# Performance work log

Hardware: AMD Instinct MI355X
Metric: run time of the kernel (lower is better)

The kernel has to match this reference:

```python
import jax, jax.numpy as jnp
import numpy as np

N, E, D = 50000, 800000, 128

def setup_inputs() -> dict:
    key = jax.random.key(0)
    ks = jax.random.split(key, 10)
    s = 0.05
    return {
        "h": jax.random.normal(ks[0], (N, D), dtype=jnp.float32),
        "coords": jax.random.normal(ks[1], (N, 3), dtype=jnp.float32),
        "edge_index": jax.random.randint(ks[2], (2, E), 0, N, dtype=jnp.int64),
        "W1": jax.random.normal(ks[3], (D, 2 * D + 1), dtype=jnp.float32) * s,
        "b1": jnp.zeros((D,), dtype=jnp.float32),
        "W2": jax.random.normal(ks[4], (D, D), dtype=jnp.float32) * s,
        "b2": jnp.zeros((D,), dtype=jnp.float32),
        "U1": jax.random.normal(ks[5], (D, 2 * D), dtype=jnp.float32) * s,
        "c1": jnp.zeros((D,), dtype=jnp.float32),
        "U2": jax.random.normal(ks[6], (D, D), dtype=jnp.float32) * s,
        "c2": jnp.zeros((D,), dtype=jnp.float32),
    }


def reference(h, coords, edge_index, W1, b1, W2, b2, U1, c1, U2, c2):
    sender, receiver = edge_index[0], edge_index[1]
    # gather endpoints
    rel = coords[sender] - coords[receiver]                  # [E, 3]
    dist = jnp.linalg.norm(rel, axis=1, keepdims=True)       # [E, 1]
    m_in = jnp.concatenate([h[sender], h[receiver], dist], axis=1)  # [E, 2D+1]
    # message MLP (Linear -> SiLU -> Linear -> SiLU)
    m = jax.nn.silu(m_in @ W1.T + b1)
    m = jax.nn.silu(m @ W2.T + b2)                           # [E, D]
    # scatter-add aggregate into receivers
    agg = jax.ops.segment_sum(m, receiver, num_segments=h.shape[0])  # [N, D]
    # update MLP (Linear -> SiLU -> Linear) with residual
    u_in = jnp.concatenate([h, agg], axis=1)                 # [N, 2D]
    u = jax.nn.silu(u_in @ U1.T + c1)
    u = u @ U2.T + c2
    return h + u
```

## Files before the change

### kernel.cpp

```cpp
#include <hip/hip_runtime.h>
#include <hip/hip_bf16.h>

#define NN 50000
#define EE 800000
#define DD 128
#define NTILES_MAX 100000

typedef __attribute__((ext_vector_type(8))) short bf16x8;
typedef __attribute__((ext_vector_type(4))) float f32x4;

__device__ __forceinline__ short f2bf(float f) {
    __hip_bfloat16 h = __float2bfloat16(f);
    return __builtin_bit_cast(short, h);
}

__device__ __forceinline__ float bf2f(short s) {
    unsigned int u = ((unsigned int)(unsigned short)s) << 16;
    return __builtin_bit_cast(float, u);
}

__device__ __forceinline__ float fast_silu(float x) {
    return x * __builtin_amdgcn_rcpf(1.0f + __expf(-x));
}

__device__ __forceinline__ bf16x8 load_frag_f32(const float* p) {
    f32x4 a = *(const f32x4*)p;
    f32x4 b = *(const f32x4*)(p + 4);
    bf16x8 t;
    t[0] = f2bf(a[0]); t[1] = f2bf(a[1]); t[2] = f2bf(a[2]); t[3] = f2bf(a[3]);
    t[4] = f2bf(b[0]); t[5] = f2bf(b[1]); t[6] = f2bf(b[2]); t[7] = f2bf(b[3]);
    return t;
}

__global__ void prep_all_kernel(const int* __restrict__ ei, int* __restrict__ cnt,
                                const float* __restrict__ W1, const float* __restrict__ W2,
                                const float* __restrict__ U1, const float* __restrict__ U2,
                                unsigned short* __restrict__ packs,
                                float* __restrict__ w1c_out) {
    if (blockIdx.x < 3125) {
        int e = blockIdx.x * 256 + threadIdx.x;
        atomicAdd(&cnt[ei[EE + e]], 1);
        return;
    }
    int t = (blockIdx.x - 3125) * blockDim.x + threadIdx.x;
    if (t >= 98304) {
        if (t < 98432) { int d = t - 98304; w1c_out[d] = W1[d * 257 + 256]; }
        return;
    }
    int mat = t >> 14;
    int r = t & 16383;
    int j = r & 7;
    int lane = (r >> 3) & 63;
    int f = r >> 9;
    int ks = f & 3, nt = f >> 2;
    int n = nt * 16 + (lane & 15);
    int k = ks * 32 + (lane >> 4) * 8 + j;
    float v;
    switch (mat) {
        case 0: v = W1[n * 257 + k];        break;
        case 1: v = W1[n * 257 + 128 + k];  break;
        case 2: v = W2[n * 128 + k];        break;
        case 3: v = U1[n * 256 + k];        break;
        case 4: v = U1[n * 256 + 128 + k];  break;
        default: v = U2[n * 128 + k];       break;
    }
    packs[t] = (unsigned short)f2bf(v);
}

__global__ void alloc_kernel(const int* __restrict__ cnt, int* __restrict__ tileCtr,
                             int* __restrict__ cursor, int2* __restrict__ tinfo,
                             float4* __restrict__ agg4) {
    int i = blockIdx.x * 256 + threadIdx.x;
    if (i >= NN) return;
    int c = cnt[i];
    int ntt = (c + 15) >> 4;
    if (ntt == 0) ntt = 1;
    int tb = atomicAdd(tileCtr, ntt);
    int base = tb << 4;
    cursor[i] = base;
    int end = base + c;
    if (ntt == 1) {
        tinfo[tb] = make_int2(i | (int)0x80000000, end);
    } else {
        for (int k = 0; k < ntt; k++) tinfo[tb + k] = make_int2(i, end);
        float4* row = agg4 + (size_t)i * 32;
        #pragma unroll 8
        for (int k = 0; k < 32; k++) row[k] = make_float4(0.f, 0.f, 0.f, 0.f);
    }
}

__global__ __launch_bounds__(256, 2) void prep_g_scatter_kernel(
    const float* __restrict__ h,
    const bf16x8* __restrict__ w1a_pack,
    const bf16x8* __restrict__ w1b_pack,
    const float* __restrict__ b1,
    unsigned short* __restrict__ G,
    const int* __restrict__ ei,
    int* __restrict__ cursor,
    int* __restrict__ ssr)
{
    if (blockIdx.x >= 782) {
        int e = (blockIdx.x - 782) * 256 + threadIdx.x;
        int s = ei[e], r = ei[EE + e];
        int pos = atomicAdd(&cursor[r], 1);
        ssr[pos] = s;
        return;
    }
    const int tid = threadIdx.x;
    const int wave = tid >> 6, lane = tid & 63;
    const int quad = lane >> 4, l15 = lane & 15;
    const int nbase = blockIdx.x * 64 + wave * 16;

    int n = nbase + l15;
    int nrow = n < NN ? n : NN - 1;

    bf16x8 ah[4];
    #pragma unroll
    for (int ks = 0; ks < 4; ks++)
        ah[ks] = load_frag_f32(h + (size_t)nrow * DD + ks * 32 + quad * 8);

    f32x4 acca[8], accb[8];
    #pragma unroll
    for (int nt = 0; nt < 8; nt++) {
        acca[nt] = f32x4{0.f, 0.f, 0.f, 0.f};
        accb[nt] = f32x4{0.f, 0.f, 0.f, 0.f};
    }

    #pragma unroll
    for (int ks = 0; ks < 4; ks++) {
        #pragma unroll
        for (int nt = 0; nt < 8; nt++)
            acca[nt] = __builtin_amdgcn_mfma_f32_16x16x32_bf16(
                ah[ks], w1a_pack[(nt * 4 + ks) * 64 + lane], acca[nt], 0, 0, 0);
        #pragma unroll
        for (int nt = 0; nt < 8; nt++)
            accb[nt] = __builtin_amdgcn_mfma_f32_16x16x32_bf16(
                ah[ks], w1b_pack[(nt * 4 + ks) * 64 + lane], accb[nt], 0, 0, 0);
    }

    #pragma unroll
    for (int nt = 0; nt < 8; nt++) {
        int d = nt * 16 + l15;
        float b1v = b1[d];
        #pragma unroll
        for (int r = 0; r < 4; r++) {
            int n2 = nbase + quad * 4 + r;
            if (n2 < NN) {
                G[(size_t)n2 * 256 + d]       = (unsigned short)f2bf(acca[nt][r] + b1v);
                G[(size_t)n2 * 256 + 128 + d] = (unsigned short)f2bf(accb[nt][r]);
            }
        }
    }
}

__global__ __launch_bounds__(256, 4) void edge_kernel(
    const unsigned short* __restrict__ G,
    const float* __restrict__ coords,
    const int* __restrict__ ssr,
    const int2* __restrict__ tinfo,
    const int* __restrict__ tileCtr,
    const bf16x8* __restrict__ w2_pack,
    const float* __restrict__ w1c,
    const float* __restrict__ b2,
    float* __restrict__ agg)
{
    __shared__ float w1c_s[4][128];

    const int tid = threadIdx.x;
    const int wave = tid >> 6, lane = tid & 63;
    const int quad = lane >> 4, l15 = lane & 15;

    w1c_s[wave][lane] = w1c[lane];
    w1c_s[wave][64 + lane] = w1c[64 + lane];
    asm volatile("s_waitcnt lgkmcnt(0)" ::: "memory");

    float b2f[8];
    #pragma unroll
    for (int nt = 0; nt < 8; nt++) b2f[nt] = b2[nt * 16 + l15];

    const int ntot = *tileCtr;
    const int tbase = (blockIdx.x * 4 + wave) * 4;

    #pragma unroll
    for (int mt = 0; mt < 4; mt++) {
        const int t = tbase + mt;
        if (t >= ntot) continue;

        const int2 ti = tinfo[t];
        const bool single = ti.x < 0;
        const int rnode = ti.x & 0x7FFFFFFF;
        const int end = ti.y;
        const int slot0 = t * 16;
        const bool fullt = (slot0 + 16 <= end);

        bf16x8 gb[4];
        #pragma unroll
        for (int ks = 0; ks < 4; ks++)
            gb[ks] = *(const bf16x8*)(G + (size_t)rnode * 256 + 128 + ks * 32 + quad * 8);
        float rx = coords[3 * rnode + 0];
        float ry = coords[3 * rnode + 1];
        float rz = coords[3 * rnode + 2];

        int sraw = ssr[slot0 + l15];
        int sc = fullt ? sraw
                       : ((slot0 + l15 < end) ? sraw : rnode);

        bf16x8 ga[4];
        #pragma unroll
        for (int ks = 0; ks < 4; ks++)
            ga[ks] = *(const bf16x8*)(G + (size_t)sc * 256 + ks * 32 + quad * 8);
        float dx = coords[3 * sc + 0] - rx;
        float dy = coords[3 * sc + 1] - ry;
        float dz = coords[3 * sc + 2] - rz;
        float dist = sqrtf(dx * dx + dy * dy + dz * dz);

        bf16x8 m1f[4];
        #pragma unroll
        for (int ks = 0; ks < 4; ks++) {
            f32x4 c0 = *(const f32x4*)&w1c_s[wave][ks * 32 + quad * 8];
            f32x4 c1 = *(const f32x4*)&w1c_s[wave][ks * 32 + quad * 8 + 4];
            #pragma unroll
            for (int j = 0; j < 4; j++) {
                float pre0 = bf2f(ga[ks][j])     + bf2f(gb[ks][j])     + dist * c0[j];
                float pre1 = bf2f(ga[ks][4 + j]) + bf2f(gb[ks][4 + j]) + dist * c1[j];
                m1f[ks][j]     = f2bf(fast_silu(pre0));
                m1f[ks][4 + j] = f2bf(fast_silu(pre1));
            }
        }

        f32x4 sv[8];
        #pragma unroll
        for (int nt = 0; nt < 8; nt++) sv[nt] = f32x4{0.f, 0.f, 0.f, 0.f};
        #pragma unroll
        for (int ks = 0; ks < 4; ks++)
            #pragma unroll
            for (int nt = 0; nt < 8; nt++)
                sv[nt] = __builtin_amdgcn_mfma_f32_16x16x32_bf16(
                    m1f[ks], w2_pack[(nt * 4 + ks) * 64 + lane], sv[nt], 0, 0, 0);

        float acc[8];
        #pragma unroll
        for (int nt = 0; nt < 8; nt++) acc[nt] = 0.f;
        if (fullt) {
            #pragma unroll
            for (int nt = 0; nt < 8; nt++)
                #pragma unroll
                for (int r = 0; r < 4; r++)
                    acc[nt] += fast_silu(sv[nt][r] + b2f[nt]);
        } else {
            float mk[4];
            #pragma unroll
            for (int r = 0; r < 4; r++)
                mk[r] = (slot0 + quad * 4 + r < end) ? 1.f : 0.f;
            #pragma unroll
            for (int nt = 0; nt < 8; nt++)
                #pragma unroll
                for (int r = 0; r < 4; r++) {
                    float v = fast_silu(sv[nt][r] + b2f[nt]);
                    acc[nt] = fmaf(v, mk[r], acc[nt]);
                }
        }

        #pragma unroll
        for (int nt = 0; nt < 8; nt++) {
            float s = acc[nt];
            s += __shfl_xor(s, 16);
            s += __shfl_xor(s, 32);
            acc[nt] = s;
        }
        size_t base = (size_t)rnode * DD + l15;
        if (single) {
            agg[base + (quad * 2 + 0) * 16] = acc[quad * 2 + 0];
            agg[base + (quad * 2 + 1) * 16] = acc[quad * 2 + 1];
        } else {
            unsafeAtomicAdd(&agg[base + (quad * 2 + 0) * 16], acc[quad * 2 + 0]);
            unsafeAtomicAdd(&agg[base + (quad * 2 + 1) * 16], acc[quad * 2 + 1]);
        }
    }
}

__global__ __launch_bounds__(256, 4) void node_kernel(
    const float* __restrict__ hf,
    const float* __restrict__ agg,
    const bf16x8* __restrict__ u1a_pack,
    const bf16x8* __restrict__ u1b_pack,
    const bf16x8* __restrict__ u2_pack,
    const float* __restrict__ c1,
    const float* __restrict__ c2,
    float* __restrict__ out)
{
    __shared__ unsigned short u1s[4][16][136];

    const int tid = threadIdx.x;
    const int wave = tid >> 6, lane = tid & 63;
    const int quad = lane >> 4, l15 = lane & 15;
    const int nbase = blockIdx.x * 64 + wave * 16;

    int n = nbase + l15;
    int nrow = n < NN ? n : NN - 1;

    float c1v[8];
    #pragma unroll
    for (int nt = 0; nt < 8; nt++) c1v[nt] = c1[nt * 16 + l15];

    bf16x8 ah[4], ag[4];
    #pragma unroll
    for (int ks = 0; ks < 4; ks++) {
        ah[ks] = load_frag_f32(hf + (size_t)nrow * DD + ks * 32 + quad * 8);
        ag[ks] = load_frag_f32(agg + (size_t)nrow * DD + ks * 32 + quad * 8);
    }

    f32x4 acc[8];
    #pragma unroll
    for (int nt = 0; nt < 8; nt++) acc[nt] = f32x4{0.f, 0.f, 0.f, 0.f};

    #pragma unroll
    for (int ks = 0; ks < 4; ks++) {
        #pragma unroll
        for (int nt = 0; nt < 8; nt++)
            acc[nt] = __builtin_amdgcn_mfma_f32_16x16x32_bf16(
                ah[ks], u1a_pack[(nt * 4 + ks) * 64 + lane], acc[nt], 0, 0, 0);
        #pragma unroll
        for (int nt = 0; nt < 8; nt++)
            acc[nt] = __builtin_amdgcn_mfma_f32_16x16x32_bf16(
                ag[ks], u1b_pack[(nt * 4 + ks) * 64 + lane], acc[nt], 0, 0, 0);
    }

    #pragma unroll
    for (int nt = 0; nt < 8; nt++) {
        int d = nt * 16 + l15;
        #pragma unroll
        for (int r = 0; r < 4; r++) {
            float pre = acc[nt][r] + c1v[nt];
            u1s[wave][quad * 4 + r][d] = (unsigned short)f2bf(fast_silu(pre));
        }
    }
    asm volatile("s_waitcnt lgkmcnt(0)" ::: "memory");

    bf16x8 a2[4];
    #pragma unroll
    for (int ks = 0; ks < 4; ks++)
        a2[ks] = *(const bf16x8*)(&u1s[wave][l15][ks * 32 + quad * 8]);

    f32x4 acc2[8];
    #pragma unroll
    for (int nt = 0; nt < 8; nt++) acc2[nt] = f32x4{0.f, 0.f, 0.f, 0.f};

    #pragma unroll
    for (int ks = 0; ks < 4; ks++)
        #pragma unroll
        for (int nt = 0; nt < 8; nt++)
            acc2[nt] = __builtin_amdgcn_mfma_f32_16x16x32_bf16(
                a2[ks], u2_pack[(nt * 4 + ks) * 64 + lane], acc2[nt], 0, 0, 0);

    #pragma unroll
    for (int nt = 0; nt < 8; nt++) {
        int d = nt * 16 + l15;
        float c2v = c2[d];
        #pragma unroll
        for (int r = 0; r < 4; r++) {
            int n2 = nbase + quad * 4 + r;
            if (n2 < NN) {
                size_t idx = (size_t)n2 * DD + d;
                out[idx] = hf[idx] + acc2[nt][r] + c2v;
            }
        }
    }
}

extern "C" void kernel_launch(void* const* d_in, const int* in_sizes, int n_in,
                              void* d_out, int out_size, void* d_ws, size_t ws_size,
                              hipStream_t stream) {
    const float* h      = (const float*)d_in[0];
    const float* coords = (const float*)d_in[1];
    const int* ei       = (const int*)d_in[2];
    const float* W1 = (const float*)d_in[3];
    const float* b1 = (const float*)d_in[4];
    const float* W2 = (const float*)d_in[5];
    const float* b2 = (const float*)d_in[6];
    const float* U1 = (const float*)d_in[7];
    const float* c1 = (const float*)d_in[8];
    const float* U2 = (const float*)d_in[9];
    const float* c2 = (const float*)d_in[10];
    float* out = (float*)d_out;

    char* ws = (char*)d_ws;
    float* agg            = (float*)ws;
    unsigned short* packs = (unsigned short*)(ws + 38400000);
    float* w1c            = (float*)(ws + 38600000);
    unsigned short* G     = (unsigned short*)(ws + 38700000);
    int* cnt              = (int*)(ws + 64300000);
    int* tileCtr          = (int*)(ws + 64500000);
    int* cursor           = (int*)(ws + 64500008);
    int2* tinfo           = (int2*)(ws + 64700008);
    int* ssr              = (int*)(ws + 65500008);
    const bf16x8* w1a = (const bf16x8*)(packs);
    const bf16x8* w1b = (const bf16x8*)(packs + 16384);
    const bf16x8* w2p = (const bf16x8*)(packs + 32768);
    const bf16x8* u1a = (const bf16x8*)(packs + 49152);
    const bf16x8* u1b = (const bf16x8*)(packs + 65536);
    const bf16x8* u2p = (const bf16x8*)(packs + 81920);

    hipMemsetAsync(cnt, 0, 200004, stream);
    prep_all_kernel<<<3510, 256, 0, stream>>>(ei, cnt, W1, W2, U1, U2, packs, w1c);
    alloc_kernel<<<196, 256, 0, stream>>>(cnt, tileCtr, cursor, tinfo, (float4*)agg);
    prep_g_scatter_kernel<<<3907, 256, 0, stream>>>(h, w1a, w1b, b1, G, ei,
                                                    cursor, ssr);
    edge_kernel<<<6250, 256, 0, stream>>>(G, coords, ssr, tinfo, tileCtr,
                                          w2p, w1c, b2, agg);
    node_kernel<<<(NN + 63) / 64, 256, 0, stream>>>(h, agg, u1a, u1b, u2p, c1, c2, out);
}
```

Before: 390.5 us.

## Pack partial receiver tiles into shared tail pool to cut padded edge tiles

Each receiver's edges are split into full 16-edge tiles and a remainder. Remainders from all receivers go into a compacted (sender, receiver) pool, which is processed in dense 16-row tiles that do a segmented reduction by receiver before the atomic adds. The goal is to drop the padding waste of one partial tile per node: about 100k padded tiles become about 50k dense ones, so the edge grid halves. In exchange, tail tiles load per-row receiver features, use a serial segmented reduce with more atomics, and agg now needs a full memset instead of direct stores for single-tile nodes.

```diff
diff --git a/kernel.cpp b/kernel.cpp
--- a/kernel.cpp
+++ b/kernel.cpp
@@ -4,7 +4,6 @@
 #define NN 50000
 #define EE 800000
 #define DD 128
-#define NTILES_MAX 100000
 
 typedef __attribute__((ext_vector_type(8))) short bf16x8;
 typedef __attribute__((ext_vector_type(4))) float f32x4;
@@ -67,26 +66,19 @@
     packs[t] = (unsigned short)f2bf(v);
 }
 
-__global__ void alloc_kernel(const int* __restrict__ cnt, int* __restrict__ tileCtr,
-                             int* __restrict__ cursor, int2* __restrict__ tinfo,
-                             float4* __restrict__ agg4) {
+__global__ void alloc_kernel(const int* __restrict__ cnt, int* __restrict__ ctrs,
+                             int* __restrict__ fullbase, int* __restrict__ tailbase,
+                             int* __restrict__ tinfoA) {
     int i = blockIdx.x * 256 + threadIdx.x;
     if (i >= NN) return;
     int c = cnt[i];
-    int ntt = (c + 15) >> 4;
-    if (ntt == 0) ntt = 1;
-    int tb = atomicAdd(tileCtr, ntt);
-    int base = tb << 4;
-    cursor[i] = base;
-    int end = base + c;
-    if (ntt == 1) {
-        tinfo[tb] = make_int2(i | (int)0x80000000, end);
-    } else {
-        for (int k = 0; k < ntt; k++) tinfo[tb + k] = make_int2(i, end);
-        float4* row = agg4 + (size_t)i * 32;
-        #pragma unroll 8
-        for (int k = 0; k < 32; k++) row[k] = make_float4(0.f, 0.f, 0.f, 0.f);
-    }
+    int nf = c >> 4, tc = c & 15;
+    if (nf) {
+        int tb = atomicAdd(&ctrs[0], nf);
+        fullbase[i] = tb << 4;
+        for (int k = 0; k < nf; k++) tinfoA[tb + k] = i;
+    }
+    if (tc) tailbase[i] = atomicAdd(&ctrs[1], tc);
 }
 
 __global__ __launch_bounds__(256, 2) void prep_g_scatter_kernel(
@@ -96,14 +88,20 @@
     const float* __restrict__ b1,
     unsigned short* __restrict__ G,
     const int* __restrict__ ei,
+    const int* __restrict__ cnt,
     int* __restrict__ cursor,
-    int* __restrict__ ssr)
+    const int* __restrict__ fullbase,
+    const int* __restrict__ tailbase,
+    int* __restrict__ ssrA,
+    int2* __restrict__ pool)
 {
     if (blockIdx.x >= 782) {
         int e = (blockIdx.x - 782) * 256 + threadIdx.x;
         int s = ei[e], r = ei[EE + e];
-        int pos = atomicAdd(&cursor[r], 1);
-        ssr[pos] = s;
+        int p = atomicAdd(&cursor[r], 1);
+        int thr = cnt[r] & ~15;
+        if (p < thr) ssrA[fullbase[r] + p] = s;
+        else         pool[tailbase[r] + p - thr] = make_int2(s, r);
         return;
     }
     const int tid = threadIdx.x;
@@ -156,9 +154,10 @@
 __global__ __launch_bounds__(256, 4) void edge_kernel(
     const unsigned short* __restrict__ G,
     const float* __restrict__ coords,
-    const int* __restrict__ ssr,
-    const int2* __restrict__ tinfo,
-    const int* __restrict__ tileCtr,
+    const int* __restrict__ ssrA,
+    const int2* __restrict__ pool,
+    const int* __restrict__ tinfoA,
+    const int* __restrict__ ctrs,
     const bf16x8* __restrict__ w2_pack,
     const float* __restrict__ w1c,
     const float* __restrict__ b2,
@@ -178,41 +177,54 @@
     #pragma unroll
     for (int nt = 0; nt < 8; nt++) b2f[nt] = b2[nt * 16 + l15];
 
-    const int ntot = *tileCtr;
+    const int nfullT = ctrs[0];
+    const int ntail  = ctrs[1];
+    const int ntiles = nfullT + ((ntail + 15) >> 4);
     const int tbase = (blockIdx.x * 4 + wave) * 4;
 
     #pragma unroll
     for (int mt = 0; mt < 4; mt++) {
         const int t = tbase + mt;
-        if (t >= ntot) continue;
-
-        const int2 ti = tinfo[t];
-        const bool single = ti.x < 0;
-        const int rnode = ti.x & 0x7FFFFFFF;
-        const int end = ti.y;
-        const int slot0 = t * 16;
-        const bool fullt = (slot0 + 16 <= end);
-
-        bf16x8 gb[4];
-        #pragma unroll
-        for (int ks = 0; ks < 4; ks++)
-            gb[ks] = *(const bf16x8*)(G + (size_t)rnode * 256 + 128 + ks * 32 + quad * 8);
-        float rx = coords[3 * rnode + 0];
-        float ry = coords[3 * rnode + 1];
-        float rz = coords[3 * rnode + 2];
-
-        int sraw = ssr[slot0 + l15];
-        int sc = fullt ? sraw
-                       : ((slot0 + l15 < end) ? sraw : rnode);
-
-        bf16x8 ga[4];
-        #pragma unroll
-        for (int ks = 0; ks < 4; ks++)
-            ga[ks] = *(const bf16x8*)(G + (size_t)sc * 256 + ks * 32 + quad * 8);
-        float dx = coords[3 * sc + 0] - rx;
-        float dy = coords[3 * sc + 1] - ry;
-        float dz = coords[3 * sc + 2] - rz;
-        float dist = sqrtf(dx * dx + dy * dy + dz * dz);
+        if (t >= ntiles) continue;
+
+        const bool full = t < nfullT;
+        bf16x8 ga[4], gb[4];
+        float dist;
+        int rnode = 0;
+        int rr = 0;
+
+        if (full) {
+            rnode = tinfoA[t];
+            #pragma unroll
+            for (int ks = 0; ks < 4; ks++)
+                gb[ks] = *(const bf16x8*)(G + (size_t)rnode * 256 + 128 + ks * 32 + quad * 8);
+            float rx = coords[3 * rnode + 0];
+            float ry = coords[3 * rnode + 1];
+            float rz = coords[3 * rnode + 2];
+            int sc = ssrA[t * 16 + l15];
+            #pragma unroll
+            for (int ks = 0; ks < 4; ks++)
+                ga[ks] = *(const bf16x8*)(G + (size_t)sc * 256 + ks * 32 + quad * 8);
+            float dx = coords[3 * sc + 0] - rx;
+            float dy = coords[3 * sc + 1] - ry;
+            float dz = coords[3 * sc + 2] - rz;
+            dist = sqrtf(dx * dx + dy * dy + dz * dz);
+        } else {
+            const int pbase = (t - nfullT) * 16;
+            int slot = pbase + l15;
+            int cl = slot < ntail ? slot : ntail - 1;
+            int2 sd = pool[cl];
+            int sc = sd.x; rr = sd.y;
+            #pragma unroll
+            for (int ks = 0; ks < 4; ks++) {
+                ga[ks] = *(const bf16x8*)(G + (size_t)sc * 256 + ks * 32 + quad * 8);
+                gb[ks] = *(const bf16x8*)(G + (size_t)rr * 256 + 128 + ks * 32 + quad * 8);
+            }
+            float dx = coords[3 * sc + 0] - coords[3 * rr + 0];
+            float dy = coords[3 * sc + 1] - coords[3 * rr + 1];
+            float dz = coords[3 * sc + 2] - coords[3 * rr + 2];
+            dist = sqrtf(dx * dx + dy * dy + dz * dz);
+        }
 
         bf16x8 m1f[4];
         #pragma unroll
@@ -238,43 +250,56 @@
                 sv[nt] = __builtin_amdgcn_mfma_f32_16x16x32_bf16(
                     m1f[ks], w2_pack[(nt * 4 + ks) * 64 + lane], sv[nt], 0, 0, 0);
 
-        float acc[8];
-        #pragma unroll
-        for (int nt = 0; nt < 8; nt++) acc[nt] = 0.f;
-        if (fullt) {
-            #pragma unroll
-            for (int nt = 0; nt < 8; nt++)
+        if (full) {
+            float acc[8];
+            #pragma unroll
+            for (int nt = 0; nt < 8; nt++) {
+                float s = 0.f;
                 #pragma unroll
                 for (int r = 0; r < 4; r++)
-                    acc[nt] += fast_silu(sv[nt][r] + b2f[nt]);
+                    s += fast_silu(sv[nt][r] + b2f[nt]);
+                s += __shfl_xor(s, 16);
+                s += __shfl_xor(s, 32);
+                acc[nt] = s;
+            }
+            size_t base = (size_t)rnode * DD + l15;
+            unsafeAtomicAdd(&agg[base + (quad * 2 + 0) * 16], acc[quad * 2 + 0]);
+            unsafeAtomicAdd(&agg[base + (quad * 2 + 1) * 16], acc[quad * 2 + 1]);
         } else {
-            float mk[4];
-            #pragma unroll
-            for (int r = 0; r < 4; r++)
-                mk[r] = (slot0 + quad * 4 + r < end) ? 1.f : 0.f;
+            const int pbase = (t - nfullT) * 16;
             #pragma unroll
             for (int nt = 0; nt < 8; nt++)
                 #pragma unroll
                 for (int r = 0; r < 4; r++) {
                     float v = fast_silu(sv[nt][r] + b2f[nt]);
-                    acc[nt] = fmaf(v, mk[r], acc[nt]);
+                    sv[nt][r] = (pbase + quad * 4 + r < ntail) ? v : 0.f;
                 }
-        }
-
-        #pragma unroll
-        for (int nt = 0; nt < 8; nt++) {
-            float s = acc[nt];
-            s += __shfl_xor(s, 16);
-            s += __shfl_xor(s, 32);
-            acc[nt] = s;
-        }
-        size_t base = (size_t)rnode * DD + l15;
-        if (single) {
-            agg[base + (quad * 2 + 0) * 16] = acc[quad * 2 + 0];
-            agg[base + (quad * 2 + 1) * 16] = acc[quad * 2 + 1];
-        } else {
-            unsafeAtomicAdd(&agg[base + (quad * 2 + 0) * 16], acc[quad * 2 + 0]);
-            unsafeAtomicAdd(&agg[base + (quad * 2 + 1) * 16], acc[quad * 2 + 1]);
+            int nxt = __shfl(rr, (l15 + 1) & 15);
+            unsigned long long bal = __ballot(l15 == 15 || rr != nxt);
+            unsigned m = (unsigned)(bal & 0xFFFFull);
+            int i0 = 0;
+            while (m) {
+                int b = (int)__builtin_ctz(m);
+                m &= m - 1;
+                float tot[8];
+                #pragma unroll
+                for (int nt = 0; nt < 8; nt++) {
+                    float s = 0.f;
+                    #pragma unroll
+                    for (int r = 0; r < 4; r++) {
+                        int row = quad * 4 + r;
+                        s += (row >= i0 && row <= b) ? sv[nt][r] : 0.f;
+                    }
+                    s += __shfl_xor(s, 16);
+                    s += __shfl_xor(s, 32);
+                    tot[nt] = s;
+                }
+                int rcv = __shfl(rr, i0);
+                size_t base = (size_t)rcv * DD + l15;
+                unsafeAtomicAdd(&agg[base + (quad * 2 + 0) * 16], tot[quad * 2 + 0]);
+                unsafeAtomicAdd(&agg[base + (quad * 2 + 1) * 16], tot[quad * 2 + 1]);
+                i0 = b + 1;
+            }
         }
     }
 }
@@ -390,10 +415,13 @@
     float* w1c            = (float*)(ws + 38600000);
     unsigned short* G     = (unsigned short*)(ws + 38700000);
     int* cnt              = (int*)(ws + 64300000);
-    int* tileCtr          = (int*)(ws + 64500000);
-    int* cursor           = (int*)(ws + 64500008);
-    int2* tinfo           = (int2*)(ws + 64700008);
-    int* ssr              = (int*)(ws + 65500008);
+    int* cursor           = (int*)(ws + 64500000);
+    int* ctrs             = (int*)(ws + 64700000);
+    int* fullbase         = (int*)(ws + 64700008);
+    int* tailbase         = (int*)(ws + 64900008);
+    int* tinfoA           = (int*)(ws + 65100008);
+    int* ssrA             = (int*)(ws + 65300008);
+    int2* pool            = (int2*)(ws + 68500008);
     const bf16x8* w1a = (const bf16x8*)(packs);
     const bf16x8* w1b = (const bf16x8*)(packs + 16384);
     const bf16x8* w2p = (const bf16x8*)(packs + 32768);
@@ -401,12 +429,14 @@
     const bf16x8* u1b = (const bf16x8*)(packs + 65536);
     const bf16x8* u2p = (const bf16x8*)(packs + 81920);
 
-    hipMemsetAsync(cnt, 0, 200004, stream);
+    hipMemsetAsync(agg, 0, 25600000, stream);
+    hipMemsetAsync(cnt, 0, 400008, stream);
     prep_all_kernel<<<3510, 256, 0, stream>>>(ei, cnt, W1, W2, U1, U2, packs, w1c);
-    alloc_kernel<<<196, 256, 0, stream>>>(cnt, tileCtr, cursor, tinfo, (float4*)agg);
-    prep_g_scatter_kernel<<<3907, 256, 0, stream>>>(h, w1a, w1b, b1, G, ei,
-                                                    cursor, ssr);
-    edge_kernel<<<6250, 256, 0, stream>>>(G, coords, ssr, tinfo, tileCtr,
+    alloc_kernel<<<196, 256, 0, stream>>>(cnt, ctrs, fullbase, tailbase, tinfoA);
+    prep_g_scatter_kernel<<<3907, 256, 0, stream>>>(h, w1a, w1b, b1, G, ei, cnt,
+                                                    cursor, fullbase, tailbase,
+                                                    ssrA, pool);
+    edge_kernel<<<3126, 256, 0, stream>>>(G, coords, ssrA, pool, tinfoA, ctrs,
                                           w2p, w1c, b2, agg);
     node_kernel<<<(NN + 63) / 64, 256, 0, stream>>>(h, agg, u1a, u1b, u2p, c1, c2, out);
 }
```

New measurement: 379.1 us. -2.9%, faster.
